# Kernel tuning notes

Measured on AMD Instinct MI355X. Metric: run time of the kernel, lower is better.

The kernel has to match this reference:

```python
import jax, jax.numpy as jnp
import numpy as np

D_MODEL = 1024
NUM_HEADS = 16
HEAD_DIM = D_MODEL // NUM_HEADS
NEG_INF = -1e9


def setup_inputs() -> dict:
    key = jax.random.key(0)
    ks = jax.random.split(key, 9)
    B, S, SI = 4, 1024, 512
    scale = 1.0 / np.sqrt(D_MODEL)
    return {
        "hidden_states": jax.random.normal(ks[0], (B, S, D_MODEL), jnp.float32),
        "image_hidden_states": jax.random.normal(ks[1], (B, SI, D_MODEL), jnp.float32),
        "attention_mask": jax.random.randint(ks[2], (B, 1, S, S + SI), 0, 2, jnp.int32),
        "w_q": jax.random.normal(ks[3], (D_MODEL, D_MODEL), jnp.float32) * scale,
        "w_k": jax.random.normal(ks[4], (D_MODEL, D_MODEL), jnp.float32) * scale,
        "w_v": jax.random.normal(ks[5], (D_MODEL, D_MODEL), jnp.float32) * scale,
        "u_k": jax.random.normal(ks[6], (D_MODEL, D_MODEL), jnp.float32) * scale,
        "u_v": jax.random.normal(ks[7], (D_MODEL, D_MODEL), jnp.float32) * scale,
        "w_o": jax.random.normal(ks[8], (D_MODEL, D_MODEL), jnp.float32) * scale,
    }


def _split_heads(x):
    # [B, S, D] -> [B, H, S, Dh]
    B, S, _ = x.shape
    return x.reshape(B, S, NUM_HEADS, HEAD_DIM).transpose(0, 2, 1, 3)


def reference(hidden_states, image_hidden_states, attention_mask,
              w_q, w_k, w_v, u_k, u_v, w_o):
    # nn.Linear(bias=False): y = x @ W.T
    q = _split_heads(hidden_states @ w_q.T)          # [B,H,S,Dh]
    k = _split_heads(hidden_states @ w_k.T)          # [B,H,S,Dh]
    v = _split_heads(hidden_states @ w_v.T)
    k_img = _split_heads(image_hidden_states @ u_k.T)  # [B,H,SI,Dh]
    v_img = _split_heads(image_hidden_states @ u_v.T)
    k = jnp.concatenate([k, k_img], axis=2)          # [B,H,S+SI,Dh]
    v = jnp.concatenate([v, v_img], axis=2)

    scores = jnp.einsum('bhqd,bhkd->bhqk', q, k) / np.sqrt(HEAD_DIM)
    scores = jnp.where(attention_mask == 0, NEG_INF, scores)
    p_attn = jax.nn.softmax(scores, axis=-1)         # dropout p=0.0 (eval)
    x = jnp.einsum('bhqk,bhkd->bhqd', p_attn, v)     # [B,H,S,Dh]
    B, H, S, Dh = x.shape
    x = x.transpose(0, 2, 1, 3).reshape(B, S, D_MODEL)
    return x @ w_o.T
```

## Files before the change

kernel.cpp:

```cpp
#include <hip/hip_runtime.h>
#include <stdint.h>


typedef unsigned short u16;
typedef short bf16x8v __attribute__((ext_vector_type(8)));
typedef float f32x4 __attribute__((ext_vector_type(4)));

__device__ __forceinline__ u16 f2bf(float f) {
  union { float f; uint32_t u; } x; x.f = f;
  uint32_t r = x.u + 0x7FFFu + ((x.u >> 16) & 1u);
  return (u16)(r >> 16);
}

__device__ __forceinline__ uint32_t cvtpk(float a, float b) {
  uint32_t r;
  asm("v_cvt_pk_bf16_f32 %0, %1, %2" : "=v"(r) : "v"(a), "v"(b));
  return r;
}

__device__ __forceinline__ float maskand(float e, uint32_t msrc, int off) {
  uint32_t mm = (uint32_t)((int32_t)(msrc << (31 - off)) >> 31);
  union { float f; uint32_t u; } x; x.f = e; x.u &= mm; return x.f;
}

__device__ __forceinline__ void gl_lds16(const u16* g, u16* l) {
  __builtin_amdgcn_global_load_lds((const __attribute__((address_space(1))) unsigned int*)g,
                                   (__attribute__((address_space(3))) unsigned int*)l,
                                   16, 0, 0);
}

__global__ __launch_bounds__(256) void prep(const int* __restrict__ mk,
                                            const float4* __restrict__ hs,
                                            const float4* __restrict__ im,
                                            const float4* __restrict__ w0, const float4* __restrict__ w1,
                                            const float4* __restrict__ w2, const float4* __restrict__ w3,
                                            const float4* __restrict__ w4, const float4* __restrict__ w5,
                                            uint32_t* __restrict__ Mw,
                                            u16* __restrict__ Hb, u16* __restrict__ Ib,
                                            u16* __restrict__ Wb) {
  const int nthr = gridDim.x * 256;
  const int gid = blockIdx.x * 256 + threadIdx.x;

  for (int w = gid; w < 196608; w += nthr) {
    const int4* p = (const int4*)(mk + (size_t)w * 32);
    uint32_t bits = 0;
    #pragma unroll
    for (int c = 0; c < 8; ++c) {
      int4 v = p[c];
      bits |= (uint32_t)(v.x != 0) << (4 * c);
      bits |= (uint32_t)(v.y != 0) << (4 * c + 1);
      bits |= (uint32_t)(v.z != 0) << (4 * c + 2);
      bits |= (uint32_t)(v.w != 0) << (4 * c + 3);
    }
    Mw[w] = bits;
  }
  for (int i = gid; i < 1572864; i += nthr) {
    float4 v; u16* d;
    if (i < 1048576) { v = hs[i];            d = Hb + (size_t)i * 4; }
    else             { v = im[i - 1048576];  d = Ib + (size_t)(i - 1048576) * 4; }
    ushort4 o; o.x = f2bf(v.x); o.y = f2bf(v.y); o.z = f2bf(v.z); o.w = f2bf(v.w);
    *(ushort4*)d = o;
  }
  for (int i = gid; i < 1572864; i += nthr) {
    int w = i >> 18, off = i & 262143;
    const float4* s;
    switch (w) {
      case 0: s = w0; break; case 1: s = w1; break; case 2: s = w2; break;
      case 3: s = w3; break; case 4: s = w4; break; default: s = w5; break;
    }
    float4 v = s[off];
    ushort4 o; o.x = f2bf(v.x); o.y = f2bf(v.y); o.z = f2bf(v.z); o.w = f2bf(v.w);
    *(ushort4*)(Wb + ((size_t)w << 20) + (size_t)off * 4) = o;
  }
}

__global__ __launch_bounds__(512, 2) void gemm_qkv(const u16* __restrict__ Hb, const u16* __restrict__ Ib,
                                                   const u16* __restrict__ Wb,
                                                   u16* __restrict__ Qd, u16* __restrict__ Kd,
                                                   u16* __restrict__ Vd)
{
  __shared__ __align__(16) u16 As[2 * 16384];
  __shared__ __align__(16) u16 Bs[2 * 16384];
  const int bid = blockIdx.x;
  const u16 *A, *Bm;
  int bm, bn, mode;
  if (bid < 192) { mode = 4; A = Hb; Bm = Wb;
                   bm = (bid / 12) * 256; bn = (bid % 12) * 256; }
  else           { mode = 5; A = Ib; Bm = Wb + 3 * 1048576;
                   int r = bid - 192; bm = (r >> 3) * 256; bn = (r & 7) * 256; }
  const int tid = threadIdx.x, lane = tid & 63, wave = tid >> 6;
  const int wr = wave >> 2, wc = wave & 3;
  const int g = lane >> 4, c = lane & 15, cs = c & 7;
  const int srow = tid >> 3;
  const int pch  = tid & 7;
  const int swz  = (pch ^ (srow & 7)) * 8;

  f32x4 zf = {0.f, 0.f, 0.f, 0.f};
  f32x4 acc[8][4];
  #pragma unroll
  for (int f = 0; f < 8; ++f)
    #pragma unroll
    for (int nf = 0; nf < 4; ++nf) acc[f][nf] = zf;

  #define STG(GP, LDSA, base, buf, half, kt)                                        \
    do {                                                                            \
      _Pragma("unroll")                                                             \
      for (int j_ = 0; j_ < 2; ++j_) {                                              \
        int row_ = j_ * 64 + srow;                                                  \
        gl_lds16((GP) + (size_t)((base) + (half) * 128 + row_) * 1024 + (kt) * 64 + swz, \
                 &(LDSA)[(buf) * 16384 + (half) * 8192 + row_ * 64 + pch * 8]);     \
      }                                                                             \
    } while (0)

  STG(A,  As, bm, 0, 0, 0);
  STG(A,  As, bm, 0, 1, 0);
  STG(Bm, Bs, bn, 0, 0, 0);
  STG(Bm, Bs, bn, 0, 1, 0);

  for (int kt = 0; kt < 16; ++kt) {
    const int bc = (kt & 1) * 16384;
    const int bx = (kt + 1) & 1;
    if (kt < 15) {
      STG(A, As, bm, bx, 0, kt + 1);
      asm volatile("s_waitcnt vmcnt(2)" ::: "memory");
    } else {
      asm volatile("s_waitcnt vmcnt(0)" ::: "memory");
    }
    asm volatile("s_barrier" ::: "memory");

    bf16x8v Bf[4][2];
    #pragma unroll
    for (int nf = 0; nf < 4; ++nf)
      #pragma unroll
      for (int ks = 0; ks < 2; ++ks)
        Bf[nf][ks] = *(const bf16x8v*)&Bs[bc + (wc * 64 + nf * 16 + c) * 64 + ((ks * 4 + g) ^ cs) * 8];

    #pragma unroll
    for (int p = 0; p < 4; ++p) {
      bf16x8v Af[2][2];
      #pragma unroll
      for (int i = 0; i < 2; ++i)
        #pragma unroll
        for (int ks = 0; ks < 2; ++ks)
          Af[i][ks] = *(const bf16x8v*)&As[bc + (wr * 128 + (p * 2 + i) * 16 + c) * 64 + ((ks * 4 + g) ^ cs) * 8];
      if (kt < 15) {
        if (p == 1)      STG(A,  As, bm, bx, 1, kt + 1);
        else if (p == 2) STG(Bm, Bs, bn, bx, 0, kt + 1);
        else if (p == 3) STG(Bm, Bs, bn, bx, 1, kt + 1);
      }
      if (p > 0) asm volatile("s_barrier" ::: "memory");
      __builtin_amdgcn_s_setprio(1);
      #pragma unroll
      for (int i = 0; i < 2; ++i)
        #pragma unroll
        for (int nf = 0; nf < 4; ++nf)
          #pragma unroll
          for (int ks = 0; ks < 2; ++ks)
            acc[p * 2 + i][nf] =
              __builtin_amdgcn_mfma_f32_16x16x32_bf16(Af[i][ks], Bf[nf][ks], acc[p * 2 + i][nf], 0, 0, 0);
      __builtin_amdgcn_s_setprio(0);
      asm volatile("s_barrier" ::: "memory");
    }
  }
  #undef STG

  #pragma unroll
  for (int f = 0; f < 8; ++f) {
    #pragma unroll
    for (int nf = 0; nf < 4; ++nf) {
      #pragma unroll
      for (int j = 0; j < 4; ++j) {
        int gm = bm + wr * 128 + f * 16 + 4 * g + j;
        int gn = bn + wc * 64 + nf * 16 + c;
        float v = acc[f][nf][j];
        if (mode == 4) {
          int b_ = gm >> 10, s_ = gm & 1023;
          if (gn < 1024)      Qd[(size_t)gm * 1024 + gn] = f2bf(v * 0.18033688011112042f);
          else if (gn < 2048) Kd[(size_t)(b_ * 1536 + s_) * 1024 + (gn - 1024)] = f2bf(v);
          else                Vd[(size_t)(b_ * 1024 + (gn - 2048)) * 1536 + s_] = f2bf(v);
        } else {
          int b_ = gm >> 9, s_ = gm & 511;
          if (gn < 1024) Kd[(size_t)(b_ * 1536 + 1024 + s_) * 1024 + gn] = f2bf(v);
          else           Vd[(size_t)(b_ * 1024 + (gn - 1024)) * 1536 + 1024 + s_] = f2bf(v);
        }
      }
    }
  }
}

__global__ __launch_bounds__(256) void gemm_out(const u16* __restrict__ A, const u16* __restrict__ Bm,
                                                float* __restrict__ Cout)
{
  __shared__ __align__(16) u16 As[128 * 64];
  __shared__ __align__(16) u16 Bs[128 * 64];
  const int tid  = threadIdx.x;
  const int lane = tid & 63, wave = tid >> 6;
  const int wr = wave >> 1, wc = wave & 1;
  const int g = lane >> 4, c = lane & 15;
  const int bm = blockIdx.y * 128;
  const int bn = blockIdx.x * 128;

  f32x4 zf = {0.f, 0.f, 0.f, 0.f};
  f32x4 acc[4][4];
  #pragma unroll
  for (int mi = 0; mi < 4; ++mi)
    #pragma unroll
    for (int ni = 0; ni < 4; ++ni) acc[mi][ni] = zf;

  const int sr  = tid >> 3;
  const int pch = tid & 7;
  const int swz = (pch ^ (sr & 7)) * 8;
  const int cs  = c & 7;

  for (int k0 = 0; k0 < 1024; k0 += 64) {
    #pragma unroll
    for (int q = 0; q < 4; ++q)
      gl_lds16(A + (size_t)(bm + q * 32 + sr) * 1024 + k0 + swz, &As[(q * 32 + sr) * 64 + pch * 8]);
    #pragma unroll
    for (int q = 0; q < 4; ++q)
      gl_lds16(Bm + (size_t)(bn + q * 32 + sr) * 1024 + k0 + swz, &Bs[(q * 32 + sr) * 64 + pch * 8]);
    __syncthreads();

    #pragma unroll
    for (int ks = 0; ks < 2; ++ks) {
      bf16x8v af[4], bfr[4];
      #pragma unroll
      for (int mi = 0; mi < 4; ++mi)
        af[mi] = *(const bf16x8v*)&As[(wr * 64 + mi * 16 + c) * 64 + (((ks * 4 + g) ^ cs)) * 8];
      #pragma unroll
      for (int ni = 0; ni < 4; ++ni)
        bfr[ni] = *(const bf16x8v*)&Bs[(wc * 64 + ni * 16 + c) * 64 + (((ks * 4 + g) ^ cs)) * 8];
      #pragma unroll
      for (int mi = 0; mi < 4; ++mi)
        #pragma unroll
        for (int ni = 0; ni < 4; ++ni)
          acc[mi][ni] = __builtin_amdgcn_mfma_f32_16x16x32_bf16(af[mi], bfr[ni], acc[mi][ni], 0, 0, 0);
    }
    __syncthreads();
  }

  #pragma unroll
  for (int mi = 0; mi < 4; ++mi)
    #pragma unroll
    for (int ni = 0; ni < 4; ++ni)
      #pragma unroll
      for (int j = 0; j < 4; ++j) {
        int gm = bm + wr * 64 + mi * 16 + 4 * g + j;
        int gn = bn + wc * 64 + ni * 16 + c;
        Cout[(size_t)gm * 1024 + gn] = acc[mi][ni][j];
      }
}

__global__ __launch_bounds__(256) void attn_kernel(const u16* __restrict__ Q, const u16* __restrict__ Kc,
                                                   const u16* __restrict__ Vt,
                                                   const uint32_t* __restrict__ Mw,
                                                   u16* __restrict__ AO)
{
  const int bid = blockIdx.x;
  const int grp = bid & 63;
  const int qt  = bid >> 6;
  const int h = grp & 15, b = grp >> 4;
  const int q0 = qt * 64;
  const int tid = threadIdx.x, lane = tid & 63, wave = tid >> 6;
  const int g = lane >> 4, c = lane & 15;
  const int qw = q0 + wave * 16;

  __shared__ __align__(16) u16 Ks[64 * 64];
  __shared__ __align__(16) u16 Vs[64 * 64];
  __shared__ __align__(16) u16 Ps[4][16 * 72];

  bf16x8v qf0, qf1;
  {
    const u16* qp = Q + (size_t)(b * 1024 + qw + c) * 1024 + h * 64 + g * 8;
    qf0 = *(const bf16x8v*)qp;
    qf1 = *(const bf16x8v*)(qp + 32);
  }
  f32x4 zf = {0.f, 0.f, 0.f, 0.f};
  f32x4 O[4];
  float l = 0.f;
  #pragma unroll
  for (int dt = 0; dt < 4; ++dt) O[dt] = zf;

  const int sr  = tid >> 3;
  const int pch = tid & 7;
  const int swz = (pch ^ (sr & 7)) * 8;
  const int cs  = c & 7;
  const u16* Kbase = Kc + (size_t)(b * 1536) * 1024 + h * 64;
  const u16* Vbase = Vt + (size_t)(b * 1024 + h * 64) * 1536;
  const uint32_t* mrow = Mw + (size_t)(b * 1024 + qw + c) * 48;

  bf16x8v kr0, kr1, vr0, vr1;
  kr0 = *(const bf16x8v*)(Kbase + (size_t)sr * 1024 + pch * 8);
  kr1 = *(const bf16x8v*)(Kbase + (size_t)(32 + sr) * 1024 + pch * 8);
  vr0 = *(const bf16x8v*)(Vbase + (size_t)sr * 1536 + pch * 8);
  vr1 = *(const bf16x8v*)(Vbase + (size_t)(32 + sr) * 1536 + pch * 8);
  *(bf16x8v*)&Ks[sr * 64 + swz]        = kr0;
  *(bf16x8v*)&Ks[(32 + sr) * 64 + swz] = kr1;
  *(bf16x8v*)&Vs[sr * 64 + swz]        = vr0;
  *(bf16x8v*)&Vs[(32 + sr) * 64 + swz] = vr1;
  __syncthreads();

  for (int kt = 0; kt < 24; ++kt) {
    if (kt < 23) {
      const int ln = (kt + 1) * 64;
      kr0 = *(const bf16x8v*)(Kbase + (size_t)(ln + sr) * 1024 + pch * 8);
      kr1 = *(const bf16x8v*)(Kbase + (size_t)(ln + 32 + sr) * 1024 + pch * 8);
      vr0 = *(const bf16x8v*)(Vbase + (size_t)sr * 1536 + ln + pch * 8);
      vr1 = *(const bf16x8v*)(Vbase + (size_t)(32 + sr) * 1536 + ln + pch * 8);
    }
    uint2 mwv = *(const uint2*)(mrow + kt * 2);

    f32x4 s[4];
    __builtin_amdgcn_s_setprio(1);
    #pragma unroll
    for (int nt = 0; nt < 4; ++nt) {
      const u16* kr = &Ks[(nt * 16 + c) * 64];
      bf16x8v k0 = *(const bf16x8v*)&kr[(g ^ cs) * 8];
      bf16x8v k1 = *(const bf16x8v*)&kr[((4 + g) ^ cs) * 8];
      f32x4 z = zf;
      z = __builtin_amdgcn_mfma_f32_16x16x32_bf16(k0, qf0, z, 0, 0, 0);
      z = __builtin_amdgcn_mfma_f32_16x16x32_bf16(k1, qf1, z, 0, 0, 0);
      s[nt] = z;
    }
    __builtin_amdgcn_s_setprio(0);

    uint64_t mq = (((uint64_t)mwv.y << 32) | (uint64_t)mwv.x) >> (4 * g);
    uint32_t mlo = (uint32_t)mq, mhi = (uint32_t)(mq >> 32);
    #pragma unroll
    for (int nt = 0; nt < 4; ++nt) {
      uint32_t msrc = (nt < 2) ? mlo : mhi;
      #pragma unroll
      for (int j = 0; j < 4; ++j) {
        float e = exp2f(s[nt][j]);
        float p = maskand(e, msrc, 16 * (nt & 1) + j);
        s[nt][j] = p;
        l += p;
      }
    }

    u16* pw = &Ps[wave][0];
    #pragma unroll
    for (int nt = 0; nt < 4; ++nt) {
      uint2 pk2;
      pk2.x = cvtpk(s[nt][0], s[nt][1]);
      pk2.y = cvtpk(s[nt][2], s[nt][3]);
      *(uint2*)&pw[c * 72 + nt * 16 + g * 4] = pk2;
    }
    bf16x8v pb0 = *(const bf16x8v*)&pw[c * 72 + g * 8];
    bf16x8v pb1 = *(const bf16x8v*)&pw[c * 72 + 32 + g * 8];
    __builtin_amdgcn_s_setprio(1);
    #pragma unroll
    for (int dt = 0; dt < 4; ++dt) {
      const u16* vr = &Vs[(dt * 16 + c) * 64];
      bf16x8v v0 = *(const bf16x8v*)&vr[(g ^ cs) * 8];
      bf16x8v v1 = *(const bf16x8v*)&vr[((4 + g) ^ cs) * 8];
      O[dt] = __builtin_amdgcn_mfma_f32_16x16x32_bf16(v0, pb0, O[dt], 0, 0, 0);
      O[dt] = __builtin_amdgcn_mfma_f32_16x16x32_bf16(v1, pb1, O[dt], 0, 0, 0);
    }
    __builtin_amdgcn_s_setprio(0);

    __syncthreads();
    if (kt < 23) {
      *(bf16x8v*)&Ks[sr * 64 + swz]        = kr0;
      *(bf16x8v*)&Ks[(32 + sr) * 64 + swz] = kr1;
      *(bf16x8v*)&Vs[sr * 64 + swz]        = vr0;
      *(bf16x8v*)&Vs[(32 + sr) * 64 + swz] = vr1;
      __syncthreads();
    }
  }

  float r = l;
  r += __shfl_xor(r, 16);
  r += __shfl_xor(r, 32);
  float inv = 1.f / r;
  size_t ro = (size_t)(b * 1024 + qw + c) * 1024 + h * 64;
  #pragma unroll
  for (int dt = 0; dt < 4; ++dt) {
    uint2 st;
    st.x = cvtpk(O[dt][0] * inv, O[dt][1] * inv);
    st.y = cvtpk(O[dt][2] * inv, O[dt][3] * inv);
    *(uint2*)&AO[ro + dt * 16 + 4 * g] = st;
  }
}

extern "C" void kernel_launch(void* const* d_in, const int* in_sizes, int n_in,
                              void* d_out, int out_size, void* d_ws, size_t ws_size,
                              hipStream_t stream) {
  (void)in_sizes; (void)n_in; (void)out_size; (void)ws_size;
  const float* hs = (const float*)d_in[0];
  const float* im = (const float*)d_in[1];
  const int*   mk = (const int*)d_in[2];
  const float* wq = (const float*)d_in[3];
  const float* wk = (const float*)d_in[4];
  const float* wv = (const float*)d_in[5];
  const float* uk = (const float*)d_in[6];
  const float* uv = (const float*)d_in[7];
  const float* wo = (const float*)d_in[8];

  char* ws = (char*)d_ws;
  u16* Hb  = (u16*)(ws + 0);
  u16* Ib  = (u16*)(ws + 8388608);
  u16* Wb  = (u16*)(ws + 12582912);
  u16* Qb  = (u16*)(ws + 25165824);
  u16* Kb  = (u16*)(ws + 33554432);
  u16* Vtb = (u16*)(ws + 46137344);
  uint32_t* Mw = (uint32_t*)(ws + 58720256);

  prep<<<2048, 256, 0, stream>>>(mk, (const float4*)hs, (const float4*)im,
                                 (const float4*)wq, (const float4*)wk, (const float4*)wv,
                                 (const float4*)uk, (const float4*)uv, (const float4*)wo,
                                 Mw, Hb, Ib, Wb);
  gemm_qkv<<<256, 512, 0, stream>>>(Hb, Ib, Wb, Qb, Kb, Vtb);
  attn_kernel<<<1024, 256, 0, stream>>>(Qb, Kb, Vtb, Mw, Hb);
  gemm_out<<<dim3(8, 32), 256, 0, stream>>>(Hb, Wb + 5 * 1048576, (float*)d_out);
}
```

Measured before the change: 165.6 us.

## Simplify QKV GEMM prefetch schedule and double-buffer output projection GEMM

The fused QKV projection GEMM now issues the whole next K-tile prefetch at the top of each iteration. It uses a single barrier per K-step instead of interleaving the loads across four sub-phases with a barrier at each one. The output projection GEMM gains double-buffered LDS with async prefetch of the next tile, waitcnt-based waiting, and raised wave priority around its MFMA blocks, replacing load-then-sync-then-compute. This cuts barrier count and exposed global-load latency. The cost is more LDS in gemm_out, which may lower occupancy, and burstier load issue in the QKV kernel.

```diff
diff --git a/kernel.cpp b/kernel.cpp
--- a/kernel.cpp
+++ b/kernel.cpp
@@ -102,27 +102,30 @@
     #pragma unroll
     for (int nf = 0; nf < 4; ++nf) acc[f][nf] = zf;
 
-  #define STG(GP, LDSA, base, buf, half, kt)                                        \
+  #define STG_ALL(buf, kt)                                                          \
     do {                                                                            \
       _Pragma("unroll")                                                             \
-      for (int j_ = 0; j_ < 2; ++j_) {                                              \
+      for (int j_ = 0; j_ < 4; ++j_) {                                              \
         int row_ = j_ * 64 + srow;                                                  \
-        gl_lds16((GP) + (size_t)((base) + (half) * 128 + row_) * 1024 + (kt) * 64 + swz, \
-                 &(LDSA)[(buf) * 16384 + (half) * 8192 + row_ * 64 + pch * 8]);     \
+        gl_lds16(A + (size_t)(bm + row_) * 1024 + (kt) * 64 + swz,                  \
+                 &As[(buf) + row_ * 64 + pch * 8]);                                 \
+      }                                                                             \
+      _Pragma("unroll")                                                             \
+      for (int j_ = 0; j_ < 4; ++j_) {                                              \
+        int row_ = j_ * 64 + srow;                                                  \
+        gl_lds16(Bm + (size_t)(bn + row_) * 1024 + (kt) * 64 + swz,                 \
+                 &Bs[(buf) + row_ * 64 + pch * 8]);                                 \
       }                                                                             \
     } while (0)
 
-  STG(A,  As, bm, 0, 0, 0);
-  STG(A,  As, bm, 0, 1, 0);
-  STG(Bm, Bs, bn, 0, 0, 0);
-  STG(Bm, Bs, bn, 0, 1, 0);
+  STG_ALL(0, 0);
 
   for (int kt = 0; kt < 16; ++kt) {
     const int bc = (kt & 1) * 16384;
-    const int bx = (kt + 1) & 1;
+    const int bx = bc ^ 16384;
     if (kt < 15) {
-      STG(A, As, bm, bx, 0, kt + 1);
-      asm volatile("s_waitcnt vmcnt(2)" ::: "memory");
+      STG_ALL(bx, kt + 1);
+      asm volatile("s_waitcnt vmcnt(8)" ::: "memory");
     } else {
       asm volatile("s_waitcnt vmcnt(0)" ::: "memory");
     }
@@ -143,12 +146,6 @@
         #pragma unroll
         for (int ks = 0; ks < 2; ++ks)
           Af[i][ks] = *(const bf16x8v*)&As[bc + (wr * 128 + (p * 2 + i) * 16 + c) * 64 + ((ks * 4 + g) ^ cs) * 8];
-      if (kt < 15) {
-        if (p == 1)      STG(A,  As, bm, bx, 1, kt + 1);
-        else if (p == 2) STG(Bm, Bs, bn, bx, 0, kt + 1);
-        else if (p == 3) STG(Bm, Bs, bn, bx, 1, kt + 1);
-      }
-      if (p > 0) asm volatile("s_barrier" ::: "memory");
       __builtin_amdgcn_s_setprio(1);
       #pragma unroll
       for (int i = 0; i < 2; ++i)
@@ -159,10 +156,10 @@
             acc[p * 2 + i][nf] =
               __builtin_amdgcn_mfma_f32_16x16x32_bf16(Af[i][ks], Bf[nf][ks], acc[p * 2 + i][nf], 0, 0, 0);
       __builtin_amdgcn_s_setprio(0);
-      asm volatile("s_barrier" ::: "memory");
-    }
-  }
-  #undef STG
+    }
+    asm volatile("s_barrier" ::: "memory");
+  }
+  #undef STG_ALL
 
   #pragma unroll
   for (int f = 0; f < 8; ++f) {
@@ -191,53 +188,74 @@
 __global__ __launch_bounds__(256) void gemm_out(const u16* __restrict__ A, const u16* __restrict__ Bm,
                                                 float* __restrict__ Cout)
 {
-  __shared__ __align__(16) u16 As[128 * 64];
-  __shared__ __align__(16) u16 Bs[128 * 64];
+  __shared__ __align__(16) u16 As[2 * 8192];
+  __shared__ __align__(16) u16 Bs[2 * 8192];
   const int tid  = threadIdx.x;
   const int lane = tid & 63, wave = tid >> 6;
   const int wr = wave >> 1, wc = wave & 1;
-  const int g = lane >> 4, c = lane & 15;
+  const int g = lane >> 4, c = lane & 15, cs = c & 7;
   const int bm = blockIdx.y * 128;
   const int bn = blockIdx.x * 128;
-
-  f32x4 zf = {0.f, 0.f, 0.f, 0.f};
-  f32x4 acc[4][4];
-  #pragma unroll
-  for (int mi = 0; mi < 4; ++mi)
-    #pragma unroll
-    for (int ni = 0; ni < 4; ++ni) acc[mi][ni] = zf;
-
   const int sr  = tid >> 3;
   const int pch = tid & 7;
   const int swz = (pch ^ (sr & 7)) * 8;
-  const int cs  = c & 7;
-
-  for (int k0 = 0; k0 < 1024; k0 += 64) {
-    #pragma unroll
-    for (int q = 0; q < 4; ++q)
-      gl_lds16(A + (size_t)(bm + q * 32 + sr) * 1024 + k0 + swz, &As[(q * 32 + sr) * 64 + pch * 8]);
-    #pragma unroll
-    for (int q = 0; q < 4; ++q)
-      gl_lds16(Bm + (size_t)(bn + q * 32 + sr) * 1024 + k0 + swz, &Bs[(q * 32 + sr) * 64 + pch * 8]);
-    __syncthreads();
+
+  f32x4 zf = {0.f, 0.f, 0.f, 0.f};
+  f32x4 acc[4][4];
+  #pragma unroll
+  for (int mi = 0; mi < 4; ++mi)
+    #pragma unroll
+    for (int ni = 0; ni < 4; ++ni) acc[mi][ni] = zf;
+
+  #define STGO(buf, kt)                                                             \
+    do {                                                                            \
+      _Pragma("unroll")                                                             \
+      for (int q_ = 0; q_ < 4; ++q_) {                                              \
+        int row_ = q_ * 32 + sr;                                                    \
+        gl_lds16(A + (size_t)(bm + row_) * 1024 + (kt) * 64 + swz,                  \
+                 &As[(buf) + row_ * 64 + pch * 8]);                                 \
+      }                                                                             \
+      _Pragma("unroll")                                                             \
+      for (int q_ = 0; q_ < 4; ++q_) {                                              \
+        int row_ = q_ * 32 + sr;                                                    \
+        gl_lds16(Bm + (size_t)(bn + row_) * 1024 + (kt) * 64 + swz,                 \
+                 &Bs[(buf) + row_ * 64 + pch * 8]);                                 \
+      }                                                                             \
+    } while (0)
+
+  STGO(0, 0);
+
+  for (int kt = 0; kt < 16; ++kt) {
+    const int bc = (kt & 1) * 8192;
+    const int bx = bc ^ 8192;
+    if (kt < 15) {
+      STGO(bx, kt + 1);
+      asm volatile("s_waitcnt vmcnt(8)" ::: "memory");
+    } else {
+      asm volatile("s_waitcnt vmcnt(0)" ::: "memory");
+    }
+    asm volatile("s_barrier" ::: "memory");
 
     #pragma unroll
     for (int ks = 0; ks < 2; ++ks) {
       bf16x8v af[4], bfr[4];
       #pragma unroll
       for (int mi = 0; mi < 4; ++mi)
-        af[mi] = *(const bf16x8v*)&As[(wr * 64 + mi * 16 + c) * 64 + (((ks * 4 + g) ^ cs)) * 8];
+        af[mi] = *(const bf16x8v*)&As[bc + (wr * 64 + mi * 16 + c) * 64 + ((ks * 4 + g) ^ cs) * 8];
       #pragma unroll
       for (int ni = 0; ni < 4; ++ni)
-        bfr[ni] = *(const bf16x8v*)&Bs[(wc * 64 + ni * 16 + c) * 64 + (((ks * 4 + g) ^ cs)) * 8];
+        bfr[ni] = *(const bf16x8v*)&Bs[bc + (wc * 64 + ni * 16 + c) * 64 + ((ks * 4 + g) ^ cs) * 8];
+      __builtin_amdgcn_s_setprio(1);
       #pragma unroll
       for (int mi = 0; mi < 4; ++mi)
         #pragma unroll
         for (int ni = 0; ni < 4; ++ni)
           acc[mi][ni] = __builtin_amdgcn_mfma_f32_16x16x32_bf16(af[mi], bfr[ni], acc[mi][ni], 0, 0, 0);
-    }
-    __syncthreads();
-  }
+      __builtin_amdgcn_s_setprio(0);
+    }
+    asm volatile("s_barrier" ::: "memory");
+  }
+  #undef STGO
 
   #pragma unroll
   for (int mi = 0; mi < 4; ++mi)
```

Result: no change. 165.4 us (-0.2%).
